# Kernel tuning notes

Hardware: AMD Instinct MI355X
Metric: run time of the kernel (lower is better)

Reference implementation:

```python
import jax, jax.numpy as jnp
import numpy as np

EMBED = 8  # attention_dim

def setup_inputs() -> dict:
    key = jax.random.key(0)
    ks = jax.random.split(key, 10)
    B, S, F = 256, 512, 64
    d = EMBED
    return {
        "state_batch": jax.random.normal(ks[0], (B, S, F), dtype=jnp.float32),
        "proj_w": jax.random.normal(ks[1], (F, d), dtype=jnp.float32) / np.sqrt(F),
        "proj_b": jnp.zeros((d,), dtype=jnp.float32),
        "rotation": jax.random.normal(ks[2], (d, d), dtype=jnp.float32),
        "entangle": jax.random.normal(ks[3], (d, d), dtype=jnp.float32),
        "w1": jax.random.normal(ks[4], (d, 32), dtype=jnp.float32) / np.sqrt(d),
        "b1": jnp.zeros((32,), dtype=jnp.float32),
        "w2": jax.random.normal(ks[5], (32, 16), dtype=jnp.float32) / np.sqrt(32),
        "b2": jnp.zeros((16,), dtype=jnp.float32),
        "w3": jax.random.normal(ks[6], (16, 1), dtype=jnp.float32) / np.sqrt(16),
        "b3": jnp.zeros((1,), dtype=jnp.float32),
    }

def reference(state_batch, proj_w, proj_b, rotation, entangle, w1, b1, w2, b2, w3, b3):
    # project: [B,S,F] @ [F,d] -> [B,S,d]
    proj = state_batch @ proj_w + proj_b
    # self-attention with trainable rotation/entangle matrices
    q = proj @ rotation            # [B,S,d]
    k = proj @ entangle            # [B,S,d]
    scores = jax.nn.softmax(jnp.einsum('bsd,btd->bst', q, k) / np.sqrt(EMBED), axis=-1)
    attn_out = jnp.einsum('bst,btd->bsd', scores, proj)  # value = proj
    # 3-layer MLP head: d -> 32 -> 16 -> 1, squeeze last dim
    h = jax.nn.relu(attn_out @ w1 + b1)
    h = jax.nn.relu(h @ w2 + b2)
    out = (h @ w3 + b3).squeeze(-1)  # [B,S]
    return out
```

## Files before the change

kernel.cpp:

```cpp
#include <hip/hip_runtime.h>
#include <math.h>

#define SEQ 512
#define FDIM 64
#define D 8
#define NT 512
#define NPAIR 128
#define NQ 4
#define TQ (SEQ / NQ)

typedef float v2f __attribute__((ext_vector_type(2)));

__global__ __launch_bounds__(NT, 4) void hybrid_attn_kernel(
    const float* __restrict__ state,
    const float* __restrict__ proj_w,
    const float* __restrict__ proj_b,
    const float* __restrict__ rotation,
    const float* __restrict__ entangle,
    const float* __restrict__ w1,
    const float* __restrict__ b1,
    const float* __restrict__ w2,
    const float* __restrict__ b2,
    const float* __restrict__ w3,
    const float* __restrict__ b3,
    float* __restrict__ out)
{
    __shared__ __align__(16) float s_proj[SEQ * D];
    __shared__ __align__(16) float s_k[SEQ * D];
    __shared__ __align__(16) float s_q[256 * D];
    __shared__ __align__(16) float s_mrg[(NQ - 1) * NPAIR * 20];
    __shared__ __align__(16) float s_mm[NQ * NPAIR * 2];
    __shared__ __align__(16) float s_pw[FDIM * D];
    __shared__ float s_rot[D * D];
    __shared__ float s_ent[D * D];
    __shared__ float s_pb[D];
    __shared__ float s_w1[D * 32];
    __shared__ float s_b1[32];
    __shared__ float s_w2[32 * 16];
    __shared__ float s_b2[16];
    __shared__ float s_w3[16];
    __shared__ float s_b3[1];

    const int bb   = blockIdx.x;
    const int b    = bb >> 1;
    const int half = bb & 1;
    const int tid  = threadIdx.x;

    if (tid < FDIM * D) s_pw[tid] = proj_w[tid];
    if (tid < D * D) {
        s_rot[tid] = rotation[tid];
        s_ent[tid] = entangle[tid];
    }
    if (tid < D)       s_pb[tid] = proj_b[tid];
    if (tid < D * 32)  s_w1[tid] = w1[tid];
    if (tid < 32)      s_b1[tid] = b1[tid];
    if (tid < 32 * 16) s_w2[tid] = w2[tid];
    if (tid < 16) { s_b2[tid] = b2[tid]; s_w3[tid] = w3[tid]; }
    if (tid == 0)      s_b3[0] = b3[0];
    __syncthreads();

    {
        const int r = tid;
        float pj[D];
        #pragma unroll
        for (int j = 0; j < D; j++) pj[j] = s_pb[j];

        const float4* srp = (const float4*)(state + ((size_t)b * SEQ + r) * FDIM);
        #pragma unroll
        for (int c = 0; c < FDIM / 4; c++) {
            float4 v = srp[c];
            float vs[4] = {v.x, v.y, v.z, v.w};
            #pragma unroll
            for (int e = 0; e < 4; e++) {
                #pragma unroll
                for (int j = 0; j < D; j++) pj[j] += vs[e] * s_pw[(c * 4 + e) * D + j];
            }
        }

        const float QS = 0.35355339059327373f;
        float qv[D], kv[D];
        #pragma unroll
        for (int j = 0; j < D; j++) {
            float aq = 0.f, ak = 0.f;
            #pragma unroll
            for (int i = 0; i < D; i++) {
                aq += pj[i] * s_rot[i * D + j];
                ak += pj[i] * s_ent[i * D + j];
            }
            qv[j] = aq * QS;
            kv[j] = ak;
        }

        float4* dp = (float4*)(s_proj + r * D);
        dp[0] = make_float4(pj[0], pj[1], pj[2], pj[3]);
        dp[1] = make_float4(pj[4], pj[5], pj[6], pj[7]);
        float4* dk = (float4*)(s_k + r * D);
        dk[0] = make_float4(kv[0], kv[1], kv[2], kv[3]);
        dk[1] = make_float4(kv[4], kv[5], kv[6], kv[7]);
        if ((r >> 8) == half) {
            float4* dq = (float4*)(s_q + (r & 255) * D);
            dq[0] = make_float4(qv[0], qv[1], qv[2], qv[3]);
            dq[1] = make_float4(qv[4], qv[5], qv[6], qv[7]);
        }
    }
    __syncthreads();

    const int p    = tid & (NPAIR - 1);
    const int qt   = tid >> 7;
    const int toff = qt * TQ;

    v2f q0[4], q1[4];
    {
        const float4* qp = (const float4*)(s_q + p * D);
        float4 x0 = qp[0], x1 = qp[1];
        q0[0] = (v2f){x0.x, x0.y}; q0[1] = (v2f){x0.z, x0.w};
        q0[2] = (v2f){x1.x, x1.y}; q0[3] = (v2f){x1.z, x1.w};
        const float4* qp2 = (const float4*)(s_q + (p + NPAIR) * D);
        float4 y0 = qp2[0], y1 = qp2[1];
        q1[0] = (v2f){y0.x, y0.y}; q1[1] = (v2f){y0.z, y0.w};
        q1[2] = (v2f){y1.x, y1.y}; q1[3] = (v2f){y1.z, y1.w};
    }

    const float* kp = s_k    + toff * D;
    const float* vp = s_proj + toff * D;

    float m0 = -1e30f, m1 = -1e30f;
    for (int i = 0; i < TQ / 4; i++) {
        const float4* kt = (const float4*)(kp + (4 * i) * D);
        float4 ka = kt[0], kb = kt[1];
        v2f kk0 = (v2f){ka.x, ka.y}, kk1 = (v2f){ka.z, ka.w};
        v2f kk2 = (v2f){kb.x, kb.y}, kk3 = (v2f){kb.z, kb.w};
        v2f d0 = q0[0] * kk0; d0 = q0[1] * kk1 + d0;
        d0 = q0[2] * kk2 + d0; d0 = q0[3] * kk3 + d0;
        v2f d1 = q1[0] * kk0; d1 = q1[1] * kk1 + d1;
        d1 = q1[2] * kk2 + d1; d1 = q1[3] * kk3 + d1;
        m0 = fmaxf(m0, d0.x + d0.y);
        m1 = fmaxf(m1, d1.x + d1.y);
    }
    s_mm[(qt * NPAIR + p) * 2 + 0] = m0;
    s_mm[(qt * NPAIR + p) * 2 + 1] = m1;
    __syncthreads();
    #pragma unroll
    for (int w = 0; w < NQ; w++) {
        m0 = fmaxf(m0, s_mm[(w * NPAIR + p) * 2 + 0]);
        m1 = fmaxf(m1, s_mm[(w * NPAIR + p) * 2 + 1]);
    }
    const float nm0 = -m0, nm1 = -m1;

    float l0 = 0.f, l1 = 0.f;
    v2f acc0[4] = {(v2f){0.f,0.f},(v2f){0.f,0.f},(v2f){0.f,0.f},(v2f){0.f,0.f}};
    v2f acc1[4] = {(v2f){0.f,0.f},(v2f){0.f,0.f},(v2f){0.f,0.f},(v2f){0.f,0.f}};
    #pragma unroll 2
    for (int t = 0; t < TQ; t++) {
        const float4* kt = (const float4*)(kp + t * D);
        float4 ka = kt[0], kb = kt[1];
        v2f kk0 = (v2f){ka.x, ka.y}, kk1 = (v2f){ka.z, ka.w};
        v2f kk2 = (v2f){kb.x, kb.y}, kk3 = (v2f){kb.z, kb.w};
        const float4* vt = (const float4*)(vp + t * D);
        float4 va = vt[0], vb = vt[1];
        v2f vv0 = (v2f){va.x, va.y}, vv1 = (v2f){va.z, va.w};
        v2f vv2 = (v2f){vb.x, vb.y}, vv3 = (v2f){vb.z, vb.w};

        v2f d0 = q0[0] * kk0; d0 = q0[1] * kk1 + d0;
        d0 = q0[2] * kk2 + d0; d0 = q0[3] * kk3 + d0;
        v2f d1 = q1[0] * kk0; d1 = q1[1] * kk1 + d1;
        d1 = q1[2] * kk2 + d1; d1 = q1[3] * kk3 + d1;

        float e0 = __expf(d0.x + d0.y + nm0);
        float e1 = __expf(d1.x + d1.y + nm1);
        l0 += e0; l1 += e1;
        v2f e0v = (v2f){e0, e0}, e1v = (v2f){e1, e1};
        acc0[0] = e0v * vv0 + acc0[0]; acc0[1] = e0v * vv1 + acc0[1];
        acc0[2] = e0v * vv2 + acc0[2]; acc0[3] = e0v * vv3 + acc0[3];
        acc1[0] = e1v * vv0 + acc1[0]; acc1[1] = e1v * vv1 + acc1[1];
        acc1[2] = e1v * vv2 + acc1[2]; acc1[3] = e1v * vv3 + acc1[3];
    }
    __syncthreads();

    if (qt > 0) {
        float* dd = s_mrg + (size_t)((qt - 1) * NPAIR + p) * 20;
        ((float4*)dd)[0] = make_float4(acc0[0].x, acc0[0].y, acc0[1].x, acc0[1].y);
        ((float4*)dd)[1] = make_float4(acc0[2].x, acc0[2].y, acc0[3].x, acc0[3].y);
        ((float4*)dd)[2] = make_float4(acc1[0].x, acc1[0].y, acc1[1].x, acc1[1].y);
        ((float4*)dd)[3] = make_float4(acc1[2].x, acc1[2].y, acc1[3].x, acc1[3].y);
        dd[16] = l0;
        dd[17] = l1;
    }
    __syncthreads();

    float* const s_attn = s_q;
    if (qt == 0) {
        #pragma unroll
        for (int w = 0; w < NQ - 1; w++) {
            const float* ss = s_mrg + (size_t)(w * NPAIR + p) * 20;
            float4 u0 = ((const float4*)ss)[0], u1 = ((const float4*)ss)[1];
            float4 u2 = ((const float4*)ss)[2], u3 = ((const float4*)ss)[3];
            acc0[0] += (v2f){u0.x, u0.y}; acc0[1] += (v2f){u0.z, u0.w};
            acc0[2] += (v2f){u1.x, u1.y}; acc0[3] += (v2f){u1.z, u1.w};
            acc1[0] += (v2f){u2.x, u2.y}; acc1[1] += (v2f){u2.z, u2.w};
            acc1[2] += (v2f){u3.x, u3.y}; acc1[3] += (v2f){u3.z, u3.w};
            l0 += ss[16];
            l1 += ss[17];
        }

        const float inv0 = 1.0f / l0;
        const float inv1 = 1.0f / l1;
        float4* d0 = (float4*)(s_attn + p * D);
        d0[0] = make_float4(acc0[0].x*inv0, acc0[0].y*inv0, acc0[1].x*inv0, acc0[1].y*inv0);
        d0[1] = make_float4(acc0[2].x*inv0, acc0[2].y*inv0, acc0[3].x*inv0, acc0[3].y*inv0);
        float4* d1 = (float4*)(s_attn + (p + NPAIR) * D);
        d1[0] = make_float4(acc1[0].x*inv1, acc1[0].y*inv1, acc1[1].x*inv1, acc1[1].y*inv1);
        d1[1] = make_float4(acc1[2].x*inv1, acc1[2].y*inv1, acc1[3].x*inv1, acc1[3].y*inv1);
    }
    __syncthreads();

    if (tid < 256) {
        const float4* ap = (const float4*)(s_attn + tid * D);
        float4 a0 = ap[0], a1 = ap[1];
        float attn[D] = {a0.x, a0.y, a0.z, a0.w, a1.x, a1.y, a1.z, a1.w};

        float h1[32];
        #pragma unroll
        for (int j = 0; j < 32; j++) {
            float a = s_b1[j];
            #pragma unroll
            for (int i = 0; i < D; i++) a += attn[i] * s_w1[i * 32 + j];
            h1[j] = fmaxf(a, 0.f);
        }
        float h2[16];
        #pragma unroll
        for (int j = 0; j < 16; j++) {
            float a = s_b2[j];
            #pragma unroll
            for (int i = 0; i < 32; i++) a += h1[i] * s_w2[i * 16 + j];
            h2[j] = fmaxf(a, 0.f);
        }
        float o = s_b3[0];
        #pragma unroll
        for (int i = 0; i < 16; i++) o += h2[i] * s_w3[i];

        out[(size_t)b * SEQ + half * 256 + tid] = o;
    }
}

extern "C" void kernel_launch(void* const* d_in, const int* in_sizes, int n_in,
                              void* d_out, int out_size, void* d_ws, size_t ws_size,
                              hipStream_t stream) {
    const float* state    = (const float*)d_in[0];
    const float* proj_w   = (const float*)d_in[1];
    const float* proj_b   = (const float*)d_in[2];
    const float* rotation = (const float*)d_in[3];
    const float* entangle = (const float*)d_in[4];
    const float* w1       = (const float*)d_in[5];
    const float* b1       = (const float*)d_in[6];
    const float* w2       = (const float*)d_in[7];
    const float* b2       = (const float*)d_in[8];
    const float* w3       = (const float*)d_in[9];
    const float* b3       = (const float*)d_in[10];
    float* out = (float*)d_out;

    const int B = in_sizes[0] / (SEQ * FDIM);
    hybrid_attn_kernel<<<B * 2, NT, 0, stream>>>(
        state, proj_w, proj_b, rotation, entangle,
        w1, b1, w2, b2, w3, b3, out);
}
```

Before: 144.1 us.

## Process whole sequence per block with four queries per thread

Each block now handles a full batch element instead of half, so the projection of state (64-dim input reads and the q/k/v compute) is no longer duplicated across two blocks. Each thread processes four query rows against its key slice, amortizing the K/V shared-memory loads over more FMAs. The partial-sum merge is done in two rounds that reuse the projection buffer, to keep shared memory in check. The cost is more registers (launch bounds lowered to 2 blocks per CU) and only 256 blocks, which may underfill the 256 CUs.

```diff
diff --git a/kernel.cpp b/kernel.cpp
--- a/kernel.cpp
+++ b/kernel.cpp
@@ -5,13 +5,13 @@
 #define FDIM 64
 #define D 8
 #define NT 512
-#define NPAIR 128
+#define NP 128
 #define NQ 4
 #define TQ (SEQ / NQ)
 
 typedef float v2f __attribute__((ext_vector_type(2)));
 
-__global__ __launch_bounds__(NT, 4) void hybrid_attn_kernel(
+__global__ __launch_bounds__(NT, 2) void hybrid_attn_kernel(
     const float* __restrict__ state,
     const float* __restrict__ proj_w,
     const float* __restrict__ proj_b,
@@ -25,11 +25,9 @@
     const float* __restrict__ b3,
     float* __restrict__ out)
 {
-    __shared__ __align__(16) float s_proj[SEQ * D];
-    __shared__ __align__(16) float s_k[SEQ * D];
-    __shared__ __align__(16) float s_q[256 * D];
-    __shared__ __align__(16) float s_mrg[(NQ - 1) * NPAIR * 20];
-    __shared__ __align__(16) float s_mm[NQ * NPAIR * 2];
+    __shared__ __align__(16) float s_pv[2 * SEQ * D];
+    __shared__ __align__(16) float s_q[SEQ * D];
+    __shared__ __align__(16) float s_mm[16 * NP];
     __shared__ __align__(16) float s_pw[FDIM * D];
     __shared__ float s_rot[D * D];
     __shared__ float s_ent[D * D];
@@ -41,10 +39,11 @@
     __shared__ float s_w3[16];
     __shared__ float s_b3[1];
 
-    const int bb   = blockIdx.x;
-    const int b    = bb >> 1;
-    const int half = bb & 1;
-    const int tid  = threadIdx.x;
+    float* const s_proj = s_pv;
+    float* const s_k    = s_pv + SEQ * D;
+
+    const int b   = blockIdx.x;
+    const int tid = threadIdx.x;
 
     if (tid < FDIM * D) s_pw[tid] = proj_w[tid];
     if (tid < D * D) {
@@ -97,59 +96,62 @@
         float4* dk = (float4*)(s_k + r * D);
         dk[0] = make_float4(kv[0], kv[1], kv[2], kv[3]);
         dk[1] = make_float4(kv[4], kv[5], kv[6], kv[7]);
-        if ((r >> 8) == half) {
-            float4* dq = (float4*)(s_q + (r & 255) * D);
-            dq[0] = make_float4(qv[0], qv[1], qv[2], qv[3]);
-            dq[1] = make_float4(qv[4], qv[5], qv[6], qv[7]);
-        }
-    }
-    __syncthreads();
-
-    const int p    = tid & (NPAIR - 1);
+        float4* dq = (float4*)(s_q + r * D);
+        dq[0] = make_float4(qv[0], qv[1], qv[2], qv[3]);
+        dq[1] = make_float4(qv[4], qv[5], qv[6], qv[7]);
+    }
+    __syncthreads();
+
+    const int p    = tid & (NP - 1);
     const int qt   = tid >> 7;
     const int toff = qt * TQ;
 
-    v2f q0[4], q1[4];
-    {
-        const float4* qp = (const float4*)(s_q + p * D);
+    v2f q[4][4];
+    #pragma unroll
+    for (int u = 0; u < 4; u++) {
+        const float4* qp = (const float4*)(s_q + (p + NP * u) * D);
         float4 x0 = qp[0], x1 = qp[1];
-        q0[0] = (v2f){x0.x, x0.y}; q0[1] = (v2f){x0.z, x0.w};
-        q0[2] = (v2f){x1.x, x1.y}; q0[3] = (v2f){x1.z, x1.w};
-        const float4* qp2 = (const float4*)(s_q + (p + NPAIR) * D);
-        float4 y0 = qp2[0], y1 = qp2[1];
-        q1[0] = (v2f){y0.x, y0.y}; q1[1] = (v2f){y0.z, y0.w};
-        q1[2] = (v2f){y1.x, y1.y}; q1[3] = (v2f){y1.z, y1.w};
+        q[u][0] = (v2f){x0.x, x0.y}; q[u][1] = (v2f){x0.z, x0.w};
+        q[u][2] = (v2f){x1.x, x1.y}; q[u][3] = (v2f){x1.z, x1.w};
     }
 
     const float* kp = s_k    + toff * D;
     const float* vp = s_proj + toff * D;
 
-    float m0 = -1e30f, m1 = -1e30f;
+    float m[4] = {-1e30f, -1e30f, -1e30f, -1e30f};
     for (int i = 0; i < TQ / 4; i++) {
         const float4* kt = (const float4*)(kp + (4 * i) * D);
         float4 ka = kt[0], kb = kt[1];
         v2f kk0 = (v2f){ka.x, ka.y}, kk1 = (v2f){ka.z, ka.w};
         v2f kk2 = (v2f){kb.x, kb.y}, kk3 = (v2f){kb.z, kb.w};
-        v2f d0 = q0[0] * kk0; d0 = q0[1] * kk1 + d0;
-        d0 = q0[2] * kk2 + d0; d0 = q0[3] * kk3 + d0;
-        v2f d1 = q1[0] * kk0; d1 = q1[1] * kk1 + d1;
-        d1 = q1[2] * kk2 + d1; d1 = q1[3] * kk3 + d1;
-        m0 = fmaxf(m0, d0.x + d0.y);
-        m1 = fmaxf(m1, d1.x + d1.y);
-    }
-    s_mm[(qt * NPAIR + p) * 2 + 0] = m0;
-    s_mm[(qt * NPAIR + p) * 2 + 1] = m1;
-    __syncthreads();
-    #pragma unroll
-    for (int w = 0; w < NQ; w++) {
-        m0 = fmaxf(m0, s_mm[(w * NPAIR + p) * 2 + 0]);
-        m1 = fmaxf(m1, s_mm[(w * NPAIR + p) * 2 + 1]);
-    }
-    const float nm0 = -m0, nm1 = -m1;
-
-    float l0 = 0.f, l1 = 0.f;
-    v2f acc0[4] = {(v2f){0.f,0.f},(v2f){0.f,0.f},(v2f){0.f,0.f},(v2f){0.f,0.f}};
-    v2f acc1[4] = {(v2f){0.f,0.f},(v2f){0.f,0.f},(v2f){0.f,0.f},(v2f){0.f,0.f}};
+        #pragma unroll
+        for (int u = 0; u < 4; u++) {
+            v2f d = q[u][0] * kk0; d = q[u][1] * kk1 + d;
+            d = q[u][2] * kk2 + d; d = q[u][3] * kk3 + d;
+            m[u] = fmaxf(m[u], d.x + d.y);
+        }
+    }
+    #pragma unroll
+    for (int u = 0; u < 4; u++) s_mm[(u * 4 + qt) * NP + p] = m[u];
+    __syncthreads();
+    float nm[4];
+    #pragma unroll
+    for (int u = 0; u < 4; u++) {
+        float mu = s_mm[(u * 4 + 0) * NP + p];
+        mu = fmaxf(mu, s_mm[(u * 4 + 1) * NP + p]);
+        mu = fmaxf(mu, s_mm[(u * 4 + 2) * NP + p]);
+        mu = fmaxf(mu, s_mm[(u * 4 + 3) * NP + p]);
+        nm[u] = -mu;
+    }
+
+    float l[4] = {0.f, 0.f, 0.f, 0.f};
+    v2f acc[4][4];
+    #pragma unroll
+    for (int u = 0; u < 4; u++) {
+        #pragma unroll
+        for (int j = 0; j < 4; j++) acc[u][j] = (v2f){0.f, 0.f};
+    }
+
     #pragma unroll 2
     for (int t = 0; t < TQ; t++) {
         const float4* kt = (const float4*)(kp + t * D);
@@ -161,60 +163,68 @@
         v2f vv0 = (v2f){va.x, va.y}, vv1 = (v2f){va.z, va.w};
         v2f vv2 = (v2f){vb.x, vb.y}, vv3 = (v2f){vb.z, vb.w};
 
-        v2f d0 = q0[0] * kk0; d0 = q0[1] * kk1 + d0;
-        d0 = q0[2] * kk2 + d0; d0 = q0[3] * kk3 + d0;
-        v2f d1 = q1[0] * kk0; d1 = q1[1] * kk1 + d1;
-        d1 = q1[2] * kk2 + d1; d1 = q1[3] * kk3 + d1;
-
-        float e0 = __expf(d0.x + d0.y + nm0);
-        float e1 = __expf(d1.x + d1.y + nm1);
-        l0 += e0; l1 += e1;
-        v2f e0v = (v2f){e0, e0}, e1v = (v2f){e1, e1};
-        acc0[0] = e0v * vv0 + acc0[0]; acc0[1] = e0v * vv1 + acc0[1];
-        acc0[2] = e0v * vv2 + acc0[2]; acc0[3] = e0v * vv3 + acc0[3];
-        acc1[0] = e1v * vv0 + acc1[0]; acc1[1] = e1v * vv1 + acc1[1];
-        acc1[2] = e1v * vv2 + acc1[2]; acc1[3] = e1v * vv3 + acc1[3];
-    }
-    __syncthreads();
-
-    if (qt > 0) {
-        float* dd = s_mrg + (size_t)((qt - 1) * NPAIR + p) * 20;
-        ((float4*)dd)[0] = make_float4(acc0[0].x, acc0[0].y, acc0[1].x, acc0[1].y);
-        ((float4*)dd)[1] = make_float4(acc0[2].x, acc0[2].y, acc0[3].x, acc0[3].y);
-        ((float4*)dd)[2] = make_float4(acc1[0].x, acc1[0].y, acc1[1].x, acc1[1].y);
-        ((float4*)dd)[3] = make_float4(acc1[2].x, acc1[2].y, acc1[3].x, acc1[3].y);
-        dd[16] = l0;
-        dd[17] = l1;
-    }
-    __syncthreads();
+        float e[4];
+        #pragma unroll
+        for (int u = 0; u < 4; u++) {
+            v2f d = (v2f){nm[u], 0.f};
+            d = q[u][0] * kk0 + d; d = q[u][1] * kk1 + d;
+            d = q[u][2] * kk2 + d; d = q[u][3] * kk3 + d;
+            e[u] = __expf(d.x + d.y);
+            l[u] += e[u];
+        }
+        #pragma unroll
+        for (int u = 0; u < 4; u++) {
+            v2f ev = (v2f){e[u], e[u]};
+            acc[u][0] = ev * vv0 + acc[u][0]; acc[u][1] = ev * vv1 + acc[u][1];
+            acc[u][2] = ev * vv2 + acc[u][2]; acc[u][3] = ev * vv3 + acc[u][3];
+        }
+    }
+    __syncthreads();
+
+    float* const s_mrg = s_pv;
+    #pragma unroll
+    for (int rnd = 0; rnd < 2; rnd++) {
+        const int ua = 2 * rnd, ub = 2 * rnd + 1;
+        if (qt > 0) {
+            float* dd = s_mrg + (size_t)((qt - 1) * NP + p) * 18;
+            ((float4*)dd)[0] = make_float4(acc[ua][0].x, acc[ua][0].y, acc[ua][1].x, acc[ua][1].y);
+            ((float4*)dd)[1] = make_float4(acc[ua][2].x, acc[ua][2].y, acc[ua][3].x, acc[ua][3].y);
+            ((float4*)dd)[2] = make_float4(acc[ub][0].x, acc[ub][0].y, acc[ub][1].x, acc[ub][1].y);
+            ((float4*)dd)[3] = make_float4(acc[ub][2].x, acc[ub][2].y, acc[ub][3].x, acc[ub][3].y);
+            dd[16] = l[ua];
+            dd[17] = l[ub];
+        }
+        __syncthreads();
+        if (qt == 0) {
+            #pragma unroll
+            for (int w = 0; w < NQ - 1; w++) {
+                const float* ss = s_mrg + (size_t)(w * NP + p) * 18;
+                float4 u0 = ((const float4*)ss)[0], u1 = ((const float4*)ss)[1];
+                float4 u2 = ((const float4*)ss)[2], u3 = ((const float4*)ss)[3];
+                acc[ua][0] += (v2f){u0.x, u0.y}; acc[ua][1] += (v2f){u0.z, u0.w};
+                acc[ua][2] += (v2f){u1.x, u1.y}; acc[ua][3] += (v2f){u1.z, u1.w};
+                acc[ub][0] += (v2f){u2.x, u2.y}; acc[ub][1] += (v2f){u2.z, u2.w};
+                acc[ub][2] += (v2f){u3.x, u3.y}; acc[ub][3] += (v2f){u3.z, u3.w};
+                l[ua] += ss[16];
+                l[ub] += ss[17];
+            }
+        }
+        __syncthreads();
+    }
 
     float* const s_attn = s_q;
     if (qt == 0) {
         #pragma unroll
-        for (int w = 0; w < NQ - 1; w++) {
-            const float* ss = s_mrg + (size_t)(w * NPAIR + p) * 20;
-            float4 u0 = ((const float4*)ss)[0], u1 = ((const float4*)ss)[1];
-            float4 u2 = ((const float4*)ss)[2], u3 = ((const float4*)ss)[3];
-            acc0[0] += (v2f){u0.x, u0.y}; acc0[1] += (v2f){u0.z, u0.w};
-            acc0[2] += (v2f){u1.x, u1.y}; acc0[3] += (v2f){u1.z, u1.w};
-            acc1[0] += (v2f){u2.x, u2.y}; acc1[1] += (v2f){u2.z, u2.w};
-            acc1[2] += (v2f){u3.x, u3.y}; acc1[3] += (v2f){u3.z, u3.w};
-            l0 += ss[16];
-            l1 += ss[17];
-        }
-
-        const float inv0 = 1.0f / l0;
-        const float inv1 = 1.0f / l1;
-        float4* d0 = (float4*)(s_attn + p * D);
-        d0[0] = make_float4(acc0[0].x*inv0, acc0[0].y*inv0, acc0[1].x*inv0, acc0[1].y*inv0);
-        d0[1] = make_float4(acc0[2].x*inv0, acc0[2].y*inv0, acc0[3].x*inv0, acc0[3].y*inv0);
-        float4* d1 = (float4*)(s_attn + (p + NPAIR) * D);
-        d1[0] = make_float4(acc1[0].x*inv1, acc1[0].y*inv1, acc1[1].x*inv1, acc1[1].y*inv1);
-        d1[1] = make_float4(acc1[2].x*inv1, acc1[2].y*inv1, acc1[3].x*inv1, acc1[3].y*inv1);
-    }
-    __syncthreads();
-
-    if (tid < 256) {
+        for (int u = 0; u < 4; u++) {
+            const float inv = 1.0f / l[u];
+            float4* dd = (float4*)(s_attn + (p + NP * u) * D);
+            dd[0] = make_float4(acc[u][0].x*inv, acc[u][0].y*inv, acc[u][1].x*inv, acc[u][1].y*inv);
+            dd[1] = make_float4(acc[u][2].x*inv, acc[u][2].y*inv, acc[u][3].x*inv, acc[u][3].y*inv);
+        }
+    }
+    __syncthreads();
+
+    {
         const float4* ap = (const float4*)(s_attn + tid * D);
         float4 a0 = ap[0], a1 = ap[1];
         float attn[D] = {a0.x, a0.y, a0.z, a0.w, a1.x, a1.y, a1.z, a1.w};
@@ -239,7 +249,7 @@
         #pragma unroll
         for (int i = 0; i < 16; i++) o += h2[i] * s_w3[i];
 
-        out[(size_t)b * SEQ + half * 256 + tid] = o;
+        out[(size_t)b * SEQ + tid] = o;
     }
 }
 
@@ -260,7 +270,7 @@
     float* out = (float*)d_out;
 
     const int B = in_sizes[0] / (SEQ * FDIM);
-    hybrid_attn_kernel<<<B * 2, NT, 0, stream>>>(
+    hybrid_attn_kernel<<<B, NT, 0, stream>>>(
         state, proj_w, proj_b, rotation, entangle,
         w1, b1, w2, b2, w3, b3, out);
 }
```

New measurement: 131.2 us. 8.9% less time.
